# Kernel optimization log

Hardware: AMD Instinct MI355X
Metric: run time of the kernel (lower is better)

Reference implementation:

```python
import jax, jax.numpy as jnp
import numpy as np

NEG = -10000.0
PAD_ID = 0


def setup_inputs() -> dict:
    key = jax.random.key(0)
    ks = jax.random.split(key, 9)
    B, S, D, K, L = 32, 256, 512, 8, 64
    word_rep = jax.random.normal(ks[0], (B, S, D), jnp.float32)
    mask = jnp.ones((B, S), jnp.int32)
    # conv_w[k,:,:,:k+1] are the taps of Conv1d(D, D, k+1); padded to width K for a single tensor
    conv_w = jax.random.normal(ks[1], (K, D, D, K), jnp.float32) * 0.02
    conv_b = jax.random.normal(ks[2], (K, D), jnp.float32) * 0.02
    cls_w = jax.random.normal(ks[3], (L, D), jnp.float32) * 0.02
    cls_b = jax.random.normal(ks[4], (L,), jnp.float32) * 0.02
    T = jax.random.normal(ks[5], (L, L), jnp.float32) * 0.01
    T = T.at[PAD_ID, :].set(NEG).at[:, PAD_ID].set(NEG)
    T_from_BEGIN = jax.random.normal(ks[6], (L,), jnp.float32) * 0.01
    T_from_BEGIN = T_from_BEGIN.at[PAD_ID].set(NEG)
    T_to_END = jax.random.normal(ks[7], (L,), jnp.float32) * 0.01
    T_to_END = T_to_END.at[PAD_ID].set(NEG)
    return dict(word_rep=word_rep, mask=mask, conv_w=conv_w, conv_b=conv_b,
                cls_w=cls_w, cls_b=cls_b, T=T, T_from_BEGIN=T_from_BEGIN, T_to_END=T_to_END)


def _semicrf(word_rep, mask, conv_w, conv_b, cls_w, cls_b, T, T_from_BEGIN, T_to_END):
    B, S, D = word_rep.shape
    K = conv_w.shape[0]
    L = cls_w.shape[0]
    # ---- segment representations: Conv1d(D, D, k+1) placed at [:, k:, k, :] ----
    x = jnp.transpose(word_rep, (0, 2, 1))  # [B, D, S]
    word_seq_rep = jnp.zeros((B, S, K, D), word_rep.dtype)
    for k in range(K):
        w = conv_w[k, :, :, :k + 1]  # [D_out, D_in, k+1]
        out = jax.lax.conv_general_dilated(
            x, w, window_strides=(1,), padding='VALID',
            dimension_numbers=('NCH', 'OIH', 'NCH')) + conv_b[k][None, :, None]  # [B, D, S-k]
        word_seq_rep = word_seq_rep.at[:, k:, k, :].set(jnp.transpose(out, (0, 2, 1)))
    # ---- label scores ----
    label_score = jnp.einsum('bskd,ld->bskl', word_seq_rep, cls_w) + cls_b  # [B,S,K,L]
    label_score = label_score.at[..., PAD_ID].set(NEG)
    seg_ok = jnp.arange(K)[None, :] <= jnp.arange(S)[:, None]  # [S, K]: segment of len k+1 valid only if t >= k
    mask3 = (mask[:, :, None] == 1) & seg_ok[None]              # [B, S, K]
    label_score = jnp.where(mask3[..., None], label_score, NEG)
    # ---- semi-CRF forward recursion over t (sequential scan) ----
    # buf[:, j] holds log_alpha at position t-1-j for j in [0, K)
    def step(buf, inp):
        ls_t, m_t, t = inp  # [B,K,L], [B,K], scalar
        lse_prev = jax.nn.logsumexp(buf, axis=2)                                  # over kk -> [B,K,L']
        tmp = jax.nn.logsumexp(T[None, None, :, :] + lse_prev[:, :, None, :], axis=3)  # over l' -> [B,K,L]
        rec = jnp.where(m_t[..., None], ls_t + tmp, NEG)
        begin = ls_t + T_from_BEGIN[None, None, :]
        karr = jnp.arange(K)[None, :, None]
        row = jnp.where(karr == t, begin, jnp.where(karr > t, NEG, rec))  # [B,K,L]
        buf = jnp.concatenate([row[:, None], buf[:, :-1]], axis=1)
        return buf, row

    buf0 = jnp.full((B, K, K, L), NEG, word_rep.dtype)
    xs = (jnp.transpose(label_score, (1, 0, 2, 3)), jnp.transpose(mask3, (1, 0, 2)), jnp.arange(S))
    _, rows = jax.lax.scan(step, buf0, xs)
    log_alpha = jnp.concatenate(
        [jnp.transpose(rows, (1, 0, 2, 3)), jnp.full((B, 1, K, L), NEG, word_rep.dtype)], axis=1)  # [B,S+1,K,L]
    # ---- log partition: gather log_alpha at last token per segment length, add T_to_END, logsumexp ----
    lengths = jnp.sum(mask, axis=1)                                   # [B]
    idxs = lengths[:, None] - (jnp.arange(K)[None, :] + 1)            # [B,K]
    idxs = jnp.where(idxs >= 0, idxs, S - 1)
    idx_arr = jnp.broadcast_to(idxs[:, None, :, None], (B, 1, K, L))
    g = jnp.take_along_axis(log_alpha, idx_arr, axis=1)[:, 0]         # [B,K,L]
    scores = g + T_to_END[None, None, :]
    return jax.nn.logsumexp(scores.reshape(B, K * L), axis=1)         # [B]


def reference(word_rep, mask, conv_w, conv_b, cls_w, cls_b, T, T_from_BEGIN, T_to_END):
    return _semicrf(word_rep, mask, conv_w, conv_b, cls_w, cls_b, T, T_from_BEGIN, T_to_END)
```

## Files before the change

### kernel.cpp

```cpp
#include <hip/hip_runtime.h>
#include <hip/hip_bf16.h>

#define NEGV (-10000.0f)
constexpr int B_ = 32, S_ = 256, D_ = 512, K_ = 8, L_ = 64;

typedef __bf16 bf16_t;
typedef bf16_t bf16x8 __attribute__((ext_vector_type(8)));
typedef float f32x4 __attribute__((ext_vector_type(4)));

__device__ __forceinline__ float u2f(unsigned int u) {
  union { unsigned int u; float f; } x; x.u = u; return x.f;
}
__device__ __forceinline__ unsigned int f2bfbits(float f) {
  union { bf16_t h; unsigned short u; } x; x.h = (bf16_t)f; return (unsigned int)x.u;
}

__global__ __launch_bounds__(256) void cast_kernel(const float* __restrict__ wr,
                                                   bf16_t* __restrict__ Awr,
                                                   const float* __restrict__ cls_w,
                                                   bf16_t* __restrict__ clsb) {
  const int bid = blockIdx.x;
  if (bid < 2048) {
    const int i = (bid * 256 + threadIdx.x) * 8;
    const float4 a = *(const float4*)(wr + i);
    const float4 b = *(const float4*)(wr + i + 4);
    bf16x8 o;
    o[0] = (bf16_t)a.x; o[1] = (bf16_t)a.y; o[2] = (bf16_t)a.z; o[3] = (bf16_t)a.w;
    o[4] = (bf16_t)b.x; o[5] = (bf16_t)b.y; o[6] = (bf16_t)b.z; o[7] = (bf16_t)b.w;
    *(bf16x8*)(Awr + i) = o;
  } else {
    const int i = ((bid - 2048) * 256 + threadIdx.x) * 8;
    const float4 a = *(const float4*)(cls_w + i);
    const float4 b = *(const float4*)(cls_w + i + 4);
    bf16x8 o;
    o[0] = (bf16_t)a.x; o[1] = (bf16_t)a.y; o[2] = (bf16_t)a.z; o[3] = (bf16_t)a.w;
    o[4] = (bf16_t)b.x; o[5] = (bf16_t)b.y; o[6] = (bf16_t)b.z; o[7] = (bf16_t)b.w;
    *(bf16x8*)(clsb + i) = o;
  }
}

__global__ __launch_bounds__(256) void w2_kernel(const float* __restrict__ conv_w,
                                                 const bf16_t* __restrict__ clsb,
                                                 bf16_t* __restrict__ Vt) {
  const int k = blockIdx.y;
  const int m0 = blockIdx.x * 128;
  const int tid = threadIdx.x;
  const int w = tid >> 6, lane = tid & 63;
  const int wm = w & 1, wn = w >> 1;
  const int lrow = lane & 15, quad = lane >> 4;
  const float* A = conv_w + (size_t)k * 2097152;
  f32x4 acc[4][2] = {};
#pragma unroll 2
  for (int kk = 0; kk < 16; kk++) {
    const int d0 = kk * 32 + quad * 8;
    const bf16x8 b0 = *(const bf16x8*)(clsb + (wn * 32 + lrow) * 512 + kk * 32 + quad * 8);
    const bf16x8 b1 = *(const bf16x8*)(clsb + (wn * 32 + 16 + lrow) * 512 + kk * 32 + quad * 8);
#pragma unroll
    for (int mi = 0; mi < 4; mi++) {
      const int ih = m0 + wm * 64 + mi * 16 + lrow;
      const float* ap = A + (size_t)d0 * 4096 + ih;
      bf16x8 a;
      a[0] = (bf16_t)ap[0 * 4096]; a[1] = (bf16_t)ap[1 * 4096];
      a[2] = (bf16_t)ap[2 * 4096]; a[3] = (bf16_t)ap[3 * 4096];
      a[4] = (bf16_t)ap[4 * 4096]; a[5] = (bf16_t)ap[5 * 4096];
      a[6] = (bf16_t)ap[6 * 4096]; a[7] = (bf16_t)ap[7 * 4096];
      acc[mi][0] = __builtin_amdgcn_mfma_f32_16x16x32_bf16(a, b0, acc[mi][0], 0, 0, 0);
      acc[mi][1] = __builtin_amdgcn_mfma_f32_16x16x32_bf16(a, b1, acc[mi][1], 0, 0, 0);
    }
  }
#pragma unroll
  for (int mi = 0; mi < 4; mi++) {
#pragma unroll
    for (int dd = 0; dd < 4; dd++) {
      const int ih = m0 + wm * 64 + mi * 16 + quad * 4 + dd;
      const int i = ih >> 3, h = ih & 7;
      const int o = k - h;
      if (o >= 0) {
#pragma unroll
        for (int ni = 0; ni < 2; ni++) {
          const int l = wn * 32 + ni * 16 + lrow;
          Vt[(size_t)(k * 64 + l) * 4096 + o * 512 + i] = (bf16_t)acc[mi][ni][dd];
        }
      }
    }
  }
}

__global__ __launch_bounds__(256) void bias2_kernel(const float* __restrict__ conv_b,
                                                    const float* __restrict__ cls_w,
                                                    const float* __restrict__ cls_b,
                                                    float* __restrict__ bias2) {
  const int k = blockIdx.x;
  const int tid = threadIdx.x;
  const int l = tid & 63, c = tid >> 6;
  __shared__ float partb[4][64];
  float s = 0.f;
  for (int d = c * 128; d < c * 128 + 128; d++)
    s += conv_b[k * D_ + d] * cls_w[l * D_ + d];
  partb[c][l] = s;
  __syncthreads();
  if (tid < 64)
    bias2[k * 64 + tid] = cls_b[tid] + partb[0][tid] + partb[1][tid] + partb[2][tid] + partb[3][tid];
}

__global__ __launch_bounds__(256) void ls_mfma(const bf16_t* __restrict__ Awr,
                                               const bf16_t* __restrict__ Vt,
                                               const float* __restrict__ bias2,
                                               const int* __restrict__ mask,
                                               unsigned int* __restrict__ ELSd) {
  constexpr int LDA = 520;
  __shared__ __align__(16) bf16_t As[71 * LDA];
  const int tid = threadIdx.x;
  const int m0 = blockIdx.x * 64;
  const int y = blockIdx.y;
  const int w = tid >> 6, lane = tid & 63;
  const int lrow = lane & 15, quad = lane >> 4;
  const int tblA[4] = {7, 0, 5, 2}, tblB[4] = {6, 1, 4, 3};
  const int kS = (y == 0) ? tblA[w] : tblB[w];

  for (int c = tid; c < 71 * 64; c += 256) {
    const int row = c >> 6, col8 = c & 63;
    int src = m0 - 7 + row;
    if (src < 0) src = 0;
    const uint4 v = *(const uint4*)(Awr + (size_t)src * 512 + col8 * 8);
    *(uint4*)(&As[row * LDA + col8 * 8]) = v;
  }
  __syncthreads();

  f32x4 acc[4][4] = {};
  const int NJ = 16 * (kS + 1);
  const bf16_t* vbase = Vt + (size_t)(kS * 64 + lrow) * 4096 + quad * 8;
#pragma unroll 2
  for (int j = 0; j < NJ; j++) {
    const int o = j >> 4;
    const int col = (j & 15) * 32;
    bf16x8 bfr[4];
#pragma unroll
    for (int ni = 0; ni < 4; ni++)
      bfr[ni] = *(const bf16x8*)(vbase + (size_t)(ni * 16) * 4096 + j * 32);
    const int abase = (lrow + 7 - o) * LDA + col + quad * 8;
#pragma unroll
    for (int mi = 0; mi < 4; mi++) {
      const bf16x8 a = *(const bf16x8*)(&As[abase + mi * 16 * LDA]);
#pragma unroll
      for (int ni = 0; ni < 4; ni++)
        acc[mi][ni] = __builtin_amdgcn_mfma_f32_16x16x32_bf16(a, bfr[ni], acc[mi][ni], 0, 0, 0);
    }
  }

  __syncthreads();
  unsigned short* buf = (unsigned short*)As;
#pragma unroll
  for (int ni = 0; ni < 4; ni++) {
    const int l = ni * 16 + lrow;
    const float bn = bias2[kS * 64 + l];
#pragma unroll
    for (int mi = 0; mi < 4; mi++) {
#pragma unroll
      for (int d = 0; d < 4; d++) {
        const int ml = mi * 16 + quad * 4 + d;
        const int m = m0 + ml;
        const int t = m & 255;
        const bool mok = (mask[m] == 1) && (t >= kS) && (l != 0);
        const float e = mok ? __expf(acc[mi][ni][d] + bn) : 0.f;
        buf[w * 4096 + ml * 64 + l] = (unsigned short)f2bfbits(e);
      }
    }
  }
  __syncthreads();
#pragma unroll
  for (int g = 0; g < 2; g++) {
    const int plane = g * 2 + y;
    const unsigned short* lo = buf + (g * 2) * 4096;
    const unsigned short* hi = buf + (g * 2 + 1) * 4096;
#pragma unroll
    for (int it = 0; it < 16; it++) {
      const int idx = it * 256 + tid;
      const unsigned int dw = (unsigned int)lo[idx] | ((unsigned int)hi[idx] << 16);
      ELSd[((size_t)plane * 8192 + m0 + (idx >> 6)) * 64 + (idx & 63)] = dw;
    }
  }
}

__global__ __launch_bounds__(64) void dp_kernel(const float* __restrict__ T,
                                                const float* __restrict__ Tfb_g,
                                                const unsigned int* __restrict__ ELSd,
                                                float* __restrict__ Mg_lin,
                                                float* __restrict__ cs_g) {
  const int b = blockIdx.x;
  const int l = threadIdx.x;
  __shared__ __align__(16) float ebuf[64];

  f32x4 rTv[16];
#pragma unroll
  for (int jj = 0; jj < 16; jj++) {
    const float4 tv = *(const float4*)(T + l * 64 + jj * 4);
    rTv[jj][0] = __expf(tv.x);
    rTv[jj][1] = __expf(tv.y);
    rTv[jj][2] = __expf(tv.z);
    rTv[jj][3] = __expf(tv.w);
  }

  const unsigned int* e0p = ELSd + ((size_t)0 * 8192 + b * 256) * 64 + l;
  const unsigned int* e1p = ELSd + ((size_t)1 * 8192 + b * 256) * 64 + l;
  const unsigned int* e2p = ELSd + ((size_t)2 * 8192 + b * 256) * 64 + l;
  const unsigned int* e3p = ELSd + ((size_t)3 * 8192 + b * 256) * 64 + l;

  float mh0 = __expf(Tfb_g[l]);
  float mh1 = 0.f, mh2 = 0.f, mh3 = 0.f, mh4 = 0.f, mh5 = 0.f, mh6 = 0.f, mh7 = 0.f;
  float c = 0.f;
  float m4 = 0.f;
  float S_next = 0.f;

  uint4 r0 = make_uint4(e0p[0 * 64], e1p[0 * 64], e2p[0 * 64], e3p[0 * 64]);
  uint4 r1 = make_uint4(e0p[1 * 64], e1p[1 * 64], e2p[1 * 64], e3p[1 * 64]);
  uint4 r2 = make_uint4(e0p[2 * 64], e1p[2 * 64], e2p[2 * 64], e3p[2 * 64]);
  uint4 r3 = make_uint4(e0p[3 * 64], e1p[3 * 64], e2p[3 * 64], e3p[3 * 64]);

  for (int t4 = 0; t4 < 256; t4 += 4) {
#pragma unroll
    for (int u = 0; u < 4; u++) {
      const int t = t4 + u;
      if (t > 0) {
        if ((t & 3) == 0) {
          const float S = fmaxf(S_next, 1e-30f);
          const float inv = __builtin_amdgcn_rcpf(S);
          c += __logf(S);
          mh7 = mh6 * inv; mh6 = mh5 * inv; mh5 = mh4 * inv; mh4 = mh3 * inv;
          mh3 = mh2 * inv; mh2 = mh1 * inv; mh1 = mh0 * inv; mh0 = m4 * inv;
        } else {
          mh7 = mh6; mh6 = mh5; mh5 = mh4; mh4 = mh3;
          mh3 = mh2; mh2 = mh1; mh1 = mh0; mh0 = m4;
        }
      }
      const uint4 q = (u == 0) ? r0 : (u == 1) ? r1 : (u == 2) ? r2 : r3;
      const float f7 = u2f(q.x << 16), fk0 = u2f(q.x & 0xFFFF0000u);
      const float f6 = u2f(q.y << 16), fk1 = u2f(q.y & 0xFFFF0000u);
      const float f5 = u2f(q.z << 16), fk2 = u2f(q.z & 0xFFFF0000u);
      const float f4 = u2f(q.w << 16), fk3 = u2f(q.w & 0xFFFF0000u);
      const float e = ((fk0 * mh0 + fk1 * mh1) + (fk2 * mh2 + fk3 * mh3)) +
                      ((f4 * mh4 + f5 * mh5) + (f6 * mh6 + f7 * mh7));
      ebuf[l] = e;
      asm volatile("s_waitcnt lgkmcnt(0)" ::: "memory");

      {
        int nt = t + 4;
        if (nt > 255) nt = 255;
        const uint4 nv = make_uint4(e0p[(size_t)nt * 64], e1p[(size_t)nt * 64],
                                    e2p[(size_t)nt * 64], e3p[(size_t)nt * 64]);
        if (u == 0) r0 = nv; else if (u == 1) r1 = nv; else if (u == 2) r2 = nv; else r3 = nv;
      }
      if ((t & 3) == 3) {
        float pm = e;
#pragma unroll
        for (int off = 32; off > 0; off >>= 1) pm = fmaxf(pm, __shfl_xor(pm, off));
        S_next = pm;
      }

      f32x4 acc = {0.f, 0.f, 0.f, 0.f};
      const f32x4* ev = (const f32x4*)ebuf;
#pragma unroll
      for (int jj = 0; jj < 16; jj++) acc += rTv[jj] * ev[jj];
      m4 = (acc[0] + acc[1]) + (acc[2] + acc[3]);

      Mg_lin[((size_t)b * 256 + t) * 64 + l] = m4;
      if (l == 0) cs_g[b * 256 + t] = c;
    }
  }
}

__global__ __launch_bounds__(64) void final_kernel(const int* __restrict__ mask,
                                                   const float* __restrict__ Tfb_g,
                                                   const float* __restrict__ T2e_g,
                                                   const unsigned int* __restrict__ ELSd,
                                                   const float* __restrict__ Mg_lin,
                                                   const float* __restrict__ cs_g,
                                                   float* __restrict__ out) {
  const int b = blockIdx.x, lane = threadIdx.x;
  int lenp = 0;
  for (int s = lane; s < S_; s += 64) lenp += (mask[b * S_ + s] == 1) ? 1 : 0;
#pragma unroll
  for (int off = 32; off > 0; off >>= 1) lenp += __shfl_xor(lenp, off);
  const int len = lenp;
  const float t2e = T2e_g[lane];
  float vals[8];
  float mx = -3.4e38f;
#pragma unroll
  for (int k = 0; k < 8; k++) {
    int tk = len - 1 - k;
    if (tk < 0) tk = S_ - 1;
    float g;
    if (k > tk) {
      g = NEGV;
    } else {
      const int p = (k < 4) ? k : (7 - k);
      const unsigned int dw = ELSd[((size_t)p * 8192 + b * 256 + tk) * 64 + lane];
      const float elsv = (k < 4) ? u2f(dw & 0xFFFF0000u) : u2f(dw << 16);
      const float ls = (elsv > 0.f) ? __logf(elsv) : NEGV;
      if (k == tk) {
        g = ls + Tfb_g[lane];
      } else if (mask[b * S_ + tk] == 1) {
        const int u = tk - 1 - k;
        const float mlin = Mg_lin[((size_t)b * S_ + u) * 64 + lane];
        const float M = (mlin > 0.f) ? (__logf(mlin) + cs_g[b * S_ + u]) : -1e30f;
        g = ls + M;
      } else {
        g = NEGV;
      }
    }
    const float v = g + t2e;
    vals[k] = v;
    mx = fmaxf(mx, v);
  }
#pragma unroll
  for (int off = 32; off > 0; off >>= 1) mx = fmaxf(mx, __shfl_xor(mx, off));
  float s = 0.f;
#pragma unroll
  for (int k = 0; k < 8; k++) s += __expf(vals[k] - mx);
#pragma unroll
  for (int off = 32; off > 0; off >>= 1) s += __shfl_xor(s, off);
  if (lane == 0) out[b] = __logf(s) + mx;
}

extern "C" void kernel_launch(void* const* d_in, const int* in_sizes, int n_in,
                              void* d_out, int out_size, void* d_ws, size_t ws_size,
                              hipStream_t stream) {
  const float* wr     = (const float*)d_in[0];
  const int*   mask   = (const int*)d_in[1];
  const float* conv_w = (const float*)d_in[2];
  const float* conv_b = (const float*)d_in[3];
  const float* cls_w  = (const float*)d_in[4];
  const float* cls_b  = (const float*)d_in[5];
  const float* T      = (const float*)d_in[6];
  const float* Tfb    = (const float*)d_in[7];
  const float* T2e    = (const float*)d_in[8];
  float* out = (float*)d_out;

  float* ws = (float*)d_ws;
  bf16_t* Vt    = (bf16_t*)ws;
  bf16_t* Awr   = (bf16_t*)(ws + 1048576);
  float*  bias2 = ws + 3145728;
  unsigned int* ELSd = (unsigned int*)(ws + 3146240);
  float*  Mg    = ws + 5243392;
  float*  cs    = ws + 5767680;
  bf16_t* clsb  = (bf16_t*)(ws + 5775872);

  cast_kernel<<<2064, 256, 0, stream>>>(wr, Awr, cls_w, clsb);
  w2_kernel<<<dim3(32, 8), 256, 0, stream>>>(conv_w, clsb, Vt);
  bias2_kernel<<<8, 256, 0, stream>>>(conv_b, cls_w, cls_b, bias2);
  ls_mfma<<<dim3(128, 2), 256, 0, stream>>>(Awr, Vt, bias2, mask, ELSd);
  dp_kernel<<<32, 64, 0, stream>>>(T, Tfb, ELSd, Mg, cs);
  final_kernel<<<32, 64, 0, stream>>>(mask, Tfb, T2e, ELSd, Mg, cs, out);
}
```

Before: 307.4 us.

## Interleave two batch DP recurrences per wavefront to hide step latency

The semi-CRF forward recurrence kernel now processes two batch elements per 64-thread block, interleaving their per-step decode, LDS exchange, and T-matrix accumulation so that one chain's latency can overlap the other's. The grid shrinks from 32 to 16 blocks, with separate LDS buffers for each chain. This trades parallelism across compute units for instruction-level parallelism within a wave, and it raises register pressure.

Result: slower. 393.2 us (+27.9%).

```diff
diff --git a/kernel.cpp b/kernel.cpp
--- a/kernel.cpp
+++ b/kernel.cpp
@@ -182,14 +182,62 @@
   }
 }
 
-__global__ __launch_bounds__(64) void dp_kernel(const float* __restrict__ T,
-                                                const float* __restrict__ Tfb_g,
-                                                const unsigned int* __restrict__ ELSd,
-                                                float* __restrict__ Mg_lin,
-                                                float* __restrict__ cs_g) {
-  const int b = blockIdx.x;
+#define DP_SHIFT_RESCALE(P)                                                  \
+  {                                                                          \
+    const float S = fmaxf(P##S, 1e-30f);                                     \
+    const float inv = __builtin_amdgcn_rcpf(S);                              \
+    P##c += __logf(S);                                                       \
+    P##mh7 = P##mh6 * inv; P##mh6 = P##mh5 * inv;                            \
+    P##mh5 = P##mh4 * inv; P##mh4 = P##mh3 * inv;                            \
+    P##mh3 = P##mh2 * inv; P##mh2 = P##mh1 * inv;                            \
+    P##mh1 = P##mh0 * inv; P##mh0 = P##m4 * inv;                             \
+  }
+
+#define DP_SHIFT_PLAIN(P)                                                    \
+  {                                                                          \
+    P##mh7 = P##mh6; P##mh6 = P##mh5; P##mh5 = P##mh4; P##mh4 = P##mh3;      \
+    P##mh3 = P##mh2; P##mh2 = P##mh1; P##mh1 = P##mh0; P##mh0 = P##m4;       \
+  }
+
+#define DP_DECODE_WRITE(P, q, eb)                                            \
+  {                                                                          \
+    const float f7 = u2f((q).x << 16), fk0 = u2f((q).x & 0xFFFF0000u);       \
+    const float f6 = u2f((q).y << 16), fk1 = u2f((q).y & 0xFFFF0000u);       \
+    const float f5 = u2f((q).z << 16), fk2 = u2f((q).z & 0xFFFF0000u);       \
+    const float f4 = u2f((q).w << 16), fk3 = u2f((q).w & 0xFFFF0000u);       \
+    P##e = ((fk0 * P##mh0 + fk1 * P##mh1) + (fk2 * P##mh2 + fk3 * P##mh3)) + \
+           ((f4 * P##mh4 + f5 * P##mh5) + (f6 * P##mh6 + f7 * P##mh7));      \
+    (eb)[l] = P##e;                                                          \
+  }
+
+#define DP_PHASE2(P, q, eb, t, u)                                            \
+  {                                                                          \
+    int nt = (t) + 4; if (nt > 255) nt = 255;                                \
+    q = make_uint4(P##e0[(size_t)nt * 64], P##e1[(size_t)nt * 64],           \
+                   P##e2[(size_t)nt * 64], P##e3[(size_t)nt * 64]);          \
+    if ((u) == 3) {                                                          \
+      float pm = P##e;                                                       \
+      pm = fmaxf(pm, __shfl_xor(pm, 32)); pm = fmaxf(pm, __shfl_xor(pm, 16));\
+      pm = fmaxf(pm, __shfl_xor(pm, 8));  pm = fmaxf(pm, __shfl_xor(pm, 4)); \
+      pm = fmaxf(pm, __shfl_xor(pm, 2));  pm = fmaxf(pm, __shfl_xor(pm, 1)); \
+      P##S = pm;                                                             \
+    }                                                                        \
+    f32x4 acc = {0.f, 0.f, 0.f, 0.f};                                        \
+    const f32x4* ev = (const f32x4*)(eb);                                    \
+    _Pragma("unroll")                                                        \
+    for (int jj = 0; jj < 16; jj++) acc += rTv[jj] * ev[jj];                 \
+    P##m4 = (acc[0] + acc[1]) + (acc[2] + acc[3]);                           \
+    Mg_lin[((size_t)P##b * 256 + (t)) * 64 + l] = P##m4;                     \
+    if (l == 0) cs_g[P##b * 256 + (t)] = P##c;                               \
+  }
+
+__global__ __launch_bounds__(64, 1) void dp_kernel(const float* __restrict__ T,
+                                                   const float* __restrict__ Tfb_g,
+                                                   const unsigned int* __restrict__ ELSd,
+                                                   float* __restrict__ Mg_lin,
+                                                   float* __restrict__ cs_g) {
   const int l = threadIdx.x;
-  __shared__ __align__(16) float ebuf[64];
+  __shared__ __align__(16) float ebuf2[2][64];
 
   f32x4 rTv[16];
 #pragma unroll
@@ -200,72 +248,60 @@
     rTv[jj][2] = __expf(tv.z);
     rTv[jj][3] = __expf(tv.w);
   }
-
-  const unsigned int* e0p = ELSd + ((size_t)0 * 8192 + b * 256) * 64 + l;
-  const unsigned int* e1p = ELSd + ((size_t)1 * 8192 + b * 256) * 64 + l;
-  const unsigned int* e2p = ELSd + ((size_t)2 * 8192 + b * 256) * 64 + l;
-  const unsigned int* e3p = ELSd + ((size_t)3 * 8192 + b * 256) * 64 + l;
-
-  float mh0 = __expf(Tfb_g[l]);
-  float mh1 = 0.f, mh2 = 0.f, mh3 = 0.f, mh4 = 0.f, mh5 = 0.f, mh6 = 0.f, mh7 = 0.f;
-  float c = 0.f;
-  float m4 = 0.f;
-  float S_next = 0.f;
-
-  uint4 r0 = make_uint4(e0p[0 * 64], e1p[0 * 64], e2p[0 * 64], e3p[0 * 64]);
-  uint4 r1 = make_uint4(e0p[1 * 64], e1p[1 * 64], e2p[1 * 64], e3p[1 * 64]);
-  uint4 r2 = make_uint4(e0p[2 * 64], e1p[2 * 64], e2p[2 * 64], e3p[2 * 64]);
-  uint4 r3 = make_uint4(e0p[3 * 64], e1p[3 * 64], e2p[3 * 64], e3p[3 * 64]);
+  const float mh0init = __expf(Tfb_g[l]);
+
+  const int Ab = blockIdx.x;
+  const int Bb = blockIdx.x + 16;
+  const unsigned int* Ae0 = ELSd + ((size_t)0 * 8192 + Ab * 256) * 64 + l;
+  const unsigned int* Ae1 = Ae0 + (size_t)8192 * 64;
+  const unsigned int* Ae2 = Ae1 + (size_t)8192 * 64;
+  const unsigned int* Ae3 = Ae2 + (size_t)8192 * 64;
+  const unsigned int* Be0 = ELSd + ((size_t)0 * 8192 + Bb * 256) * 64 + l;
+  const unsigned int* Be1 = Be0 + (size_t)8192 * 64;
+  const unsigned int* Be2 = Be1 + (size_t)8192 * 64;
+  const unsigned int* Be3 = Be2 + (size_t)8192 * 64;
+
+  float Amh0 = mh0init, Amh1 = 0.f, Amh2 = 0.f, Amh3 = 0.f,
+        Amh4 = 0.f, Amh5 = 0.f, Amh6 = 0.f, Amh7 = 0.f;
+  float Bmh0 = mh0init, Bmh1 = 0.f, Bmh2 = 0.f, Bmh3 = 0.f,
+        Bmh4 = 0.f, Bmh5 = 0.f, Bmh6 = 0.f, Bmh7 = 0.f;
+  float Ac = 0.f, Bc = 0.f, Am4 = 0.f, Bm4 = 0.f, AS = 0.f, BS = 0.f;
+  float Ae = 0.f, Be = 0.f;
+
+  uint4 Ar0 = make_uint4(Ae0[0], Ae1[0], Ae2[0], Ae3[0]);
+  uint4 Ar1 = make_uint4(Ae0[64], Ae1[64], Ae2[64], Ae3[64]);
+  uint4 Ar2 = make_uint4(Ae0[128], Ae1[128], Ae2[128], Ae3[128]);
+  uint4 Ar3 = make_uint4(Ae0[192], Ae1[192], Ae2[192], Ae3[192]);
+  uint4 Br0 = make_uint4(Be0[0], Be1[0], Be2[0], Be3[0]);
+  uint4 Br1 = make_uint4(Be0[64], Be1[64], Be2[64], Be3[64]);
+  uint4 Br2 = make_uint4(Be0[128], Be1[128], Be2[128], Be3[128]);
+  uint4 Br3 = make_uint4(Be0[192], Be1[192], Be2[192], Be3[192]);
 
   for (int t4 = 0; t4 < 256; t4 += 4) {
-#pragma unroll
-    for (int u = 0; u < 4; u++) {
-      const int t = t4 + u;
-      if (t > 0) {
-        if ((t & 3) == 0) {
-          const float S = fmaxf(S_next, 1e-30f);
-          const float inv = __builtin_amdgcn_rcpf(S);
-          c += __logf(S);
-          mh7 = mh6 * inv; mh6 = mh5 * inv; mh5 = mh4 * inv; mh4 = mh3 * inv;
-          mh3 = mh2 * inv; mh2 = mh1 * inv; mh1 = mh0 * inv; mh0 = m4 * inv;
-        } else {
-          mh7 = mh6; mh6 = mh5; mh5 = mh4; mh4 = mh3;
-          mh3 = mh2; mh2 = mh1; mh1 = mh0; mh0 = m4;
-        }
-      }
-      const uint4 q = (u == 0) ? r0 : (u == 1) ? r1 : (u == 2) ? r2 : r3;
-      const float f7 = u2f(q.x << 16), fk0 = u2f(q.x & 0xFFFF0000u);
-      const float f6 = u2f(q.y << 16), fk1 = u2f(q.y & 0xFFFF0000u);
-      const float f5 = u2f(q.z << 16), fk2 = u2f(q.z & 0xFFFF0000u);
-      const float f4 = u2f(q.w << 16), fk3 = u2f(q.w & 0xFFFF0000u);
-      const float e = ((fk0 * mh0 + fk1 * mh1) + (fk2 * mh2 + fk3 * mh3)) +
-                      ((f4 * mh4 + f5 * mh5) + (f6 * mh6 + f7 * mh7));
-      ebuf[l] = e;
-      asm volatile("s_waitcnt lgkmcnt(0)" ::: "memory");
-
-      {
-        int nt = t + 4;
-        if (nt > 255) nt = 255;
-        const uint4 nv = make_uint4(e0p[(size_t)nt * 64], e1p[(size_t)nt * 64],
-                                    e2p[(size_t)nt * 64], e3p[(size_t)nt * 64]);
-        if (u == 0) r0 = nv; else if (u == 1) r1 = nv; else if (u == 2) r2 = nv; else r3 = nv;
-      }
-      if ((t & 3) == 3) {
-        float pm = e;
-#pragma unroll
-        for (int off = 32; off > 0; off >>= 1) pm = fmaxf(pm, __shfl_xor(pm, off));
-        S_next = pm;
-      }
-
-      f32x4 acc = {0.f, 0.f, 0.f, 0.f};
-      const f32x4* ev = (const f32x4*)ebuf;
-#pragma unroll
-      for (int jj = 0; jj < 16; jj++) acc += rTv[jj] * ev[jj];
-      m4 = (acc[0] + acc[1]) + (acc[2] + acc[3]);
-
-      Mg_lin[((size_t)b * 256 + t) * 64 + l] = m4;
-      if (l == 0) cs_g[b * 256 + t] = c;
-    }
+    if (t4 > 0) { DP_SHIFT_RESCALE(A); DP_SHIFT_RESCALE(B); }
+    DP_DECODE_WRITE(A, Ar0, ebuf2[0]);
+    DP_DECODE_WRITE(B, Br0, ebuf2[1]);
+    asm volatile("s_waitcnt lgkmcnt(0)" ::: "memory");
+    DP_PHASE2(A, Ar0, ebuf2[0], t4 + 0, 0);
+    DP_PHASE2(B, Br0, ebuf2[1], t4 + 0, 0);
+    DP_SHIFT_PLAIN(A); DP_SHIFT_PLAIN(B);
+    DP_DECODE_WRITE(A, Ar1, ebuf2[0]);
+    DP_DECODE_WRITE(B, Br1, ebuf2[1]);
+    asm volatile("s_waitcnt lgkmcnt(0)" ::: "memory");
+    DP_PHASE2(A, Ar1, ebuf2[0], t4 + 1, 1);
+    DP_PHASE2(B, Br1, ebuf2[1], t4 + 1, 1);
+    DP_SHIFT_PLAIN(A); DP_SHIFT_PLAIN(B);
+    DP_DECODE_WRITE(A, Ar2, ebuf2[0]);
+    DP_DECODE_WRITE(B, Br2, ebuf2[1]);
+    asm volatile("s_waitcnt lgkmcnt(0)" ::: "memory");
+    DP_PHASE2(A, Ar2, ebuf2[0], t4 + 2, 2);
+    DP_PHASE2(B, Br2, ebuf2[1], t4 + 2, 2);
+    DP_SHIFT_PLAIN(A); DP_SHIFT_PLAIN(B);
+    DP_DECODE_WRITE(A, Ar3, ebuf2[0]);
+    DP_DECODE_WRITE(B, Br3, ebuf2[1]);
+    asm volatile("s_waitcnt lgkmcnt(0)" ::: "memory");
+    DP_PHASE2(A, Ar3, ebuf2[0], t4 + 3, 3);
+    DP_PHASE2(B, Br3, ebuf2[1], t4 + 3, 3);
   }
 }
 
@@ -349,6 +385,6 @@
   w2_kernel<<<dim3(32, 8), 256, 0, stream>>>(conv_w, clsb, Vt);
   bias2_kernel<<<8, 256, 0, stream>>>(conv_b, cls_w, cls_b, bias2);
   ls_mfma<<<dim3(128, 2), 256, 0, stream>>>(Awr, Vt, bias2, mask, ELSd);
-  dp_kernel<<<32, 64, 0, stream>>>(T, Tfb, ELSd, Mg, cs);
+  dp_kernel<<<16, 64, 0, stream>>>(T, Tfb, ELSd, Mg, cs);
   final_kernel<<<32, 64, 0, stream>>>(mask, Tfb, T2e, ELSd, Mg, cs, out);
 }
```

## Replace LDS broadcast in DP recurrence with DPP row rotations and shuffles

Applied to the files above, without the earlier changes.

The per-timestep 64x64 matvec in the semi-CRF forward DP no longer writes the emission vector to LDS and reads it back. Each lane now obtains the other quarters via three __shfl calls and rotates values within 16-lane rows using DPP row_ror, with the exp(T) registers pre-permuted to match the rotation order. The normalizer also changes from a max-reduction to a rotation-accumulated sum, which avoids the separate xor-shuffle reduction. This aims to shorten the serial latency of each of the 256 dependent steps, at the cost of 64 DPP moves per step and a different, still valid, scaling choice.

Result: no change. 313.1 us (+1.8%).

```diff
diff --git a/kernel.cpp b/kernel.cpp
--- a/kernel.cpp
+++ b/kernel.cpp
@@ -13,6 +13,12 @@
 }
 __device__ __forceinline__ unsigned int f2bfbits(float f) {
   union { bf16_t h; unsigned short u; } x; x.h = (bf16_t)f; return (unsigned int)x.u;
+}
+__device__ __forceinline__ float row_ror1(float x) {
+  union { float f; int i; } a, r;
+  a.f = x;
+  r.i = __builtin_amdgcn_update_dpp(a.i, a.i, 0x121, 0xF, 0xF, false);
+  return r.f;
 }
 
 __global__ __launch_bounds__(256) void cast_kernel(const float* __restrict__ wr,
@@ -182,24 +188,24 @@
   }
 }
 
-__global__ __launch_bounds__(64) void dp_kernel(const float* __restrict__ T,
-                                                const float* __restrict__ Tfb_g,
-                                                const unsigned int* __restrict__ ELSd,
-                                                float* __restrict__ Mg_lin,
-                                                float* __restrict__ cs_g) {
+__global__ __launch_bounds__(64, 1) void dp_kernel(const float* __restrict__ T,
+                                                   const float* __restrict__ Tfb_g,
+                                                   const unsigned int* __restrict__ ELSd,
+                                                   float* __restrict__ Mg_lin,
+                                                   float* __restrict__ cs_g) {
   const int b = blockIdx.x;
   const int l = threadIdx.x;
-  __shared__ __align__(16) float ebuf[64];
-
-  f32x4 rTv[16];
-#pragma unroll
-  for (int jj = 0; jj < 16; jj++) {
-    const float4 tv = *(const float4*)(T + l * 64 + jj * 4);
-    rTv[jj][0] = __expf(tv.x);
-    rTv[jj][1] = __expf(tv.y);
-    rTv[jj][2] = __expf(tv.z);
-    rTv[jj][3] = __expf(tv.w);
-  }
+
+  const float* Trow = T + l * 64;
+#define TE(Q, I) __expf(Trow[((((l & 48) | ((l - (I)) & 15)) + 16 * (Q)) & 63)])
+#define MKT(VAR, Q, C) \
+  const f32x4 VAR = { TE(Q, (C)*4 + 0), TE(Q, (C)*4 + 1), TE(Q, (C)*4 + 2), TE(Q, (C)*4 + 3) };
+  MKT(tA0, 0, 0) MKT(tA1, 0, 1) MKT(tA2, 0, 2) MKT(tA3, 0, 3)
+  MKT(tB0, 1, 0) MKT(tB1, 1, 1) MKT(tB2, 1, 2) MKT(tB3, 1, 3)
+  MKT(tC0, 2, 0) MKT(tC1, 2, 1) MKT(tC2, 2, 2) MKT(tC3, 2, 3)
+  MKT(tD0, 3, 0) MKT(tD1, 3, 1) MKT(tD2, 3, 2) MKT(tD3, 3, 3)
+#undef MKT
+#undef TE
 
   const unsigned int* e0p = ELSd + ((size_t)0 * 8192 + b * 256) * 64 + l;
   const unsigned int* e1p = ELSd + ((size_t)1 * 8192 + b * 256) * 64 + l;
@@ -212,61 +218,88 @@
   float m4 = 0.f;
   float S_next = 0.f;
 
+  const int lq1 = (l + 16) & 63, lq2 = (l + 32) & 63, lq3 = (l + 48) & 63;
+
   uint4 r0 = make_uint4(e0p[0 * 64], e1p[0 * 64], e2p[0 * 64], e3p[0 * 64]);
   uint4 r1 = make_uint4(e0p[1 * 64], e1p[1 * 64], e2p[1 * 64], e3p[1 * 64]);
   uint4 r2 = make_uint4(e0p[2 * 64], e1p[2 * 64], e2p[2 * 64], e3p[2 * 64]);
   uint4 r3 = make_uint4(e0p[3 * 64], e1p[3 * 64], e2p[3 * 64], e3p[3 * 64]);
 
+#define RND(TA, TB, TC, TD, E) \
+  a0 += TA[E] * v0; a1 += TB[E] * v1; a2 += TC[E] * v2; a3 += TD[E] * v3;
+#define RNDS(TA, TB, TC, TD, E)                         \
+  a0 += TA[E] * v0; s0 += v0; a1 += TB[E] * v1; s1 += v1; \
+  a2 += TC[E] * v2; s2 += v2; a3 += TD[E] * v3; s3 += v3;
+#define ROT \
+  v0 = row_ror1(v0); v1 = row_ror1(v1); v2 = row_ror1(v2); v3 = row_ror1(v3);
+
+#define DP_STEP(U, RQ)                                                          \
+  {                                                                             \
+    const int t = t4 + (U);                                                     \
+    if ((U) == 0) {                                                             \
+      if (t4 > 0) {                                                             \
+        const float S = fmaxf(S_next, 1e-30f);                                  \
+        const float inv = __builtin_amdgcn_rcpf(S);                             \
+        c += __logf(S);                                                         \
+        mh7 = mh6 * inv; mh6 = mh5 * inv; mh5 = mh4 * inv; mh4 = mh3 * inv;     \
+        mh3 = mh2 * inv; mh2 = mh1 * inv; mh1 = mh0 * inv; mh0 = m4 * inv;      \
+      }                                                                         \
+    } else {                                                                    \
+      mh7 = mh6; mh6 = mh5; mh5 = mh4; mh4 = mh3;                               \
+      mh3 = mh2; mh2 = mh1; mh1 = mh0; mh0 = m4;                                \
+    }                                                                           \
+    const float f7 = u2f(RQ.x << 16), fk0 = u2f(RQ.x & 0xFFFF0000u);            \
+    const float f6 = u2f(RQ.y << 16), fk1 = u2f(RQ.y & 0xFFFF0000u);            \
+    const float f5 = u2f(RQ.z << 16), fk2 = u2f(RQ.z & 0xFFFF0000u);            \
+    const float f4 = u2f(RQ.w << 16), fk3 = u2f(RQ.w & 0xFFFF0000u);            \
+    const float e = ((fk0 * mh0 + fk1 * mh1) + (fk2 * mh2 + fk3 * mh3)) +       \
+                    ((f4 * mh4 + f5 * mh5) + (f6 * mh6 + f7 * mh7));            \
+    const float eb1 = __shfl(e, lq1);                                           \
+    const float eb2 = __shfl(e, lq2);                                           \
+    const float eb3 = __shfl(e, lq3);                                           \
+    {                                                                           \
+      int nt = t + 4; if (nt > 255) nt = 255;                                   \
+      RQ = make_uint4(e0p[(size_t)nt * 64], e1p[(size_t)nt * 64],               \
+                      e2p[(size_t)nt * 64], e3p[(size_t)nt * 64]);              \
+    }                                                                           \
+    float a0 = 0.f, a1 = 0.f, a2 = 0.f, a3 = 0.f;                               \
+    float v0 = e, v1 = eb1, v2 = eb2, v3 = eb3;                                 \
+    if ((U) == 3) {                                                             \
+      float s0 = 0.f, s1 = 0.f, s2 = 0.f, s3 = 0.f;                             \
+      RNDS(tA0, tB0, tC0, tD0, 0) ROT RNDS(tA0, tB0, tC0, tD0, 1) ROT           \
+      RNDS(tA0, tB0, tC0, tD0, 2) ROT RNDS(tA0, tB0, tC0, tD0, 3) ROT           \
+      RNDS(tA1, tB1, tC1, tD1, 0) ROT RNDS(tA1, tB1, tC1, tD1, 1) ROT           \
+      RNDS(tA1, tB1, tC1, tD1, 2) ROT RNDS(tA1, tB1, tC1, tD1, 3) ROT           \
+      RNDS(tA2, tB2, tC2, tD2, 0) ROT RNDS(tA2, tB2, tC2, tD2, 1) ROT           \
+      RNDS(tA2, tB2, tC2, tD2, 2) ROT RNDS(tA2, tB2, tC2, tD2, 3) ROT           \
+      RNDS(tA3, tB3, tC3, tD3, 0) ROT RNDS(tA3, tB3, tC3, tD3, 1) ROT           \
+      RNDS(tA3, tB3, tC3, tD3, 2) ROT RNDS(tA3, tB3, tC3, tD3, 3)               \
+      S_next = (s0 + s1) + (s2 + s3);                                           \
+    } else {                                                                    \
+      RND(tA0, tB0, tC0, tD0, 0) ROT RND(tA0, tB0, tC0, tD0, 1) ROT             \
+      RND(tA0, tB0, tC0, tD0, 2) ROT RND(tA0, tB0, tC0, tD0, 3) ROT             \
+      RND(tA1, tB1, tC1, tD1, 0) ROT RND(tA1, tB1, tC1, tD1, 1) ROT             \
+      RND(tA1, tB1, tC1, tD1, 2) ROT RND(tA1, tB1, tC1, tD1, 3) ROT             \
+      RND(tA2, tB2, tC2, tD2, 0) ROT RND(tA2, tB2, tC2, tD2, 1) ROT             \
+      RND(tA2, tB2, tC2, tD2, 2) ROT RND(tA2, tB2, tC2, tD2, 3) ROT             \
+      RND(tA3, tB3, tC3, tD3, 0) ROT RND(tA3, tB3, tC3, tD3, 1) ROT             \
+      RND(tA3, tB3, tC3, tD3, 2) ROT RND(tA3, tB3, tC3, tD3, 3)                 \
+    }                                                                           \
+    m4 = (a0 + a1) + (a2 + a3);                                                 \
+    Mg_lin[((size_t)b * 256 + t) * 64 + l] = m4;                                \
+    if (l == 0) cs_g[b * 256 + t] = c;                                          \
+  }
+
   for (int t4 = 0; t4 < 256; t4 += 4) {
-#pragma unroll
-    for (int u = 0; u < 4; u++) {
-      const int t = t4 + u;
-      if (t > 0) {
-        if ((t & 3) == 0) {
-          const float S = fmaxf(S_next, 1e-30f);
-          const float inv = __builtin_amdgcn_rcpf(S);
-          c += __logf(S);
-          mh7 = mh6 * inv; mh6 = mh5 * inv; mh5 = mh4 * inv; mh4 = mh3 * inv;
-          mh3 = mh2 * inv; mh2 = mh1 * inv; mh1 = mh0 * inv; mh0 = m4 * inv;
-        } else {
-          mh7 = mh6; mh6 = mh5; mh5 = mh4; mh4 = mh3;
-          mh3 = mh2; mh2 = mh1; mh1 = mh0; mh0 = m4;
-        }
-      }
-      const uint4 q = (u == 0) ? r0 : (u == 1) ? r1 : (u == 2) ? r2 : r3;
-      const float f7 = u2f(q.x << 16), fk0 = u2f(q.x & 0xFFFF0000u);
-      const float f6 = u2f(q.y << 16), fk1 = u2f(q.y & 0xFFFF0000u);
-      const float f5 = u2f(q.z << 16), fk2 = u2f(q.z & 0xFFFF0000u);
-      const float f4 = u2f(q.w << 16), fk3 = u2f(q.w & 0xFFFF0000u);
-      const float e = ((fk0 * mh0 + fk1 * mh1) + (fk2 * mh2 + fk3 * mh3)) +
-                      ((f4 * mh4 + f5 * mh5) + (f6 * mh6 + f7 * mh7));
-      ebuf[l] = e;
-      asm volatile("s_waitcnt lgkmcnt(0)" ::: "memory");
-
-      {
-        int nt = t + 4;
-        if (nt > 255) nt = 255;
-        const uint4 nv = make_uint4(e0p[(size_t)nt * 64], e1p[(size_t)nt * 64],
-                                    e2p[(size_t)nt * 64], e3p[(size_t)nt * 64]);
-        if (u == 0) r0 = nv; else if (u == 1) r1 = nv; else if (u == 2) r2 = nv; else r3 = nv;
-      }
-      if ((t & 3) == 3) {
-        float pm = e;
-#pragma unroll
-        for (int off = 32; off > 0; off >>= 1) pm = fmaxf(pm, __shfl_xor(pm, off));
-        S_next = pm;
-      }
-
-      f32x4 acc = {0.f, 0.f, 0.f, 0.f};
-      const f32x4* ev = (const f32x4*)ebuf;
-#pragma unroll
-      for (int jj = 0; jj < 16; jj++) acc += rTv[jj] * ev[jj];
-      m4 = (acc[0] + acc[1]) + (acc[2] + acc[3]);
-
-      Mg_lin[((size_t)b * 256 + t) * 64 + l] = m4;
-      if (l == 0) cs_g[b * 256 + t] = c;
-    }
-  }
+    DP_STEP(0, r0)
+    DP_STEP(1, r1)
+    DP_STEP(2, r2)
+    DP_STEP(3, r3)
+  }
+#undef DP_STEP
+#undef RND
+#undef RNDS
+#undef ROT
 }
 
 __global__ __launch_bounds__(64) void final_kernel(const int* __restrict__ mask,
```

## Restructure DP recurrence to shorten serial chain and fold bias kernel into w2

Applied to the files above, without the earlier changes.

The serial per-batch DP loop is reordered so the partial dot product for the next step's emission term is computed ahead of time. Only the newest m4 term then sits on the critical path. The per-block max-shuffle reduction used for rescaling becomes a sum over the shared ebuf, computed during the same LDS reads, and the explicit lgkmcnt wait is dropped. The bias2 kernel is merged into w2_kernel (block x==0) to save one launch. Rescaling by sum instead of max changes numerics slightly, and removing the explicit wait relies on compiler ordering of the LDS write and read.

New measurement: 288.0 us. 6.3% less time.

```diff
diff --git a/kernel.cpp b/kernel.cpp
--- a/kernel.cpp
+++ b/kernel.cpp
@@ -41,7 +41,11 @@
 
 __global__ __launch_bounds__(256) void w2_kernel(const float* __restrict__ conv_w,
                                                  const bf16_t* __restrict__ clsb,
-                                                 bf16_t* __restrict__ Vt) {
+                                                 bf16_t* __restrict__ Vt,
+                                                 const float* __restrict__ conv_b,
+                                                 const float* __restrict__ cls_w,
+                                                 const float* __restrict__ cls_b,
+                                                 float* __restrict__ bias2) {
   const int k = blockIdx.y;
   const int m0 = blockIdx.x * 128;
   const int tid = threadIdx.x;
@@ -84,23 +88,17 @@
       }
     }
   }
-}
-
-__global__ __launch_bounds__(256) void bias2_kernel(const float* __restrict__ conv_b,
-                                                    const float* __restrict__ cls_w,
-                                                    const float* __restrict__ cls_b,
-                                                    float* __restrict__ bias2) {
-  const int k = blockIdx.x;
-  const int tid = threadIdx.x;
-  const int l = tid & 63, c = tid >> 6;
-  __shared__ float partb[4][64];
-  float s = 0.f;
-  for (int d = c * 128; d < c * 128 + 128; d++)
-    s += conv_b[k * D_ + d] * cls_w[l * D_ + d];
-  partb[c][l] = s;
-  __syncthreads();
-  if (tid < 64)
-    bias2[k * 64 + tid] = cls_b[tid] + partb[0][tid] + partb[1][tid] + partb[2][tid] + partb[3][tid];
+  if (blockIdx.x == 0) {
+    __shared__ float partb[4][64];
+    const int bl = tid & 63, bc = tid >> 6;
+    float s = 0.f;
+    for (int d = bc * 128; d < bc * 128 + 128; d++)
+      s += conv_b[k * D_ + d] * cls_w[bl * D_ + d];
+    partb[bc][bl] = s;
+    __syncthreads();
+    if (tid < 64)
+      bias2[k * 64 + tid] = cls_b[tid] + partb[0][tid] + partb[1][tid] + partb[2][tid] + partb[3][tid];
+  }
 }
 
 __global__ __launch_bounds__(256) void ls_mfma(const bf16_t* __restrict__ Awr,
@@ -217,56 +215,73 @@
   uint4 r2 = make_uint4(e0p[2 * 64], e1p[2 * 64], e2p[2 * 64], e3p[2 * 64]);
   uint4 r3 = make_uint4(e0p[3 * 64], e1p[3 * 64], e2p[3 * 64], e3p[3 * 64]);
 
+  float e = u2f(r0.x & 0xFFFF0000u) * mh0;
+
+#define DP_STEP(U, RQ, RN)                                                      \
+  {                                                                             \
+    const int t = t4 + (U);                                                     \
+    ebuf[l] = e;                                                                \
+                    \
+    const float nf7 = u2f(RN.x << 16), nk0 = u2f(RN.x & 0xFFFF0000u);           \
+    const float nf6 = u2f(RN.y << 16), nk1 = u2f(RN.y & 0xFFFF0000u);           \
+    const float nf5 = u2f(RN.z << 16), nk2 = u2f(RN.z & 0xFFFF0000u);           \
+    const float nf4 = u2f(RN.w << 16), nk3 = u2f(RN.w & 0xFFFF0000u);           \
+    const float pe = ((nk1 * mh0 + nk2 * mh1) + (nk3 * mh2 + nf4 * mh3)) +      \
+                     ((nf5 * mh4 + nf6 * mh5) + nf7 * mh6);                     \
+                                                  \
+    {                                                                           \
+      int nt = t + 4; if (nt > 255) nt = 255;                                   \
+      RQ = make_uint4(e0p[(size_t)nt * 64], e1p[(size_t)nt * 64],               \
+                      e2p[(size_t)nt * 64], e3p[(size_t)nt * 64]);              \
+    }                                                                           \
+                                     \
+    const f32x4* ev = (const f32x4*)ebuf;                                       \
+    f32x4 A0 = {0.f, 0.f, 0.f, 0.f}, A1 = {0.f, 0.f, 0.f, 0.f};                 \
+    f32x4 A2 = {0.f, 0.f, 0.f, 0.f}, A3 = {0.f, 0.f, 0.f, 0.f};                 \
+    if ((U) == 3) {                                                             \
+      f32x4 s0 = {0.f, 0.f, 0.f, 0.f}, s1 = {0.f, 0.f, 0.f, 0.f};               \
+      _Pragma("unroll")                                                         \
+      for (int jj = 0; jj < 4; jj++) {                                          \
+        const f32x4 v0 = ev[jj], v1 = ev[4 + jj], v2 = ev[8 + jj], v3 = ev[12 + jj]; \
+        A0 += rTv[jj] * v0; A1 += rTv[4 + jj] * v1;                             \
+        A2 += rTv[8 + jj] * v2; A3 += rTv[12 + jj] * v3;                        \
+        s0 += v0 + v2; s1 += v1 + v3;                                           \
+      }                                                                         \
+      const f32x4 ss = s0 + s1;                                                 \
+      S_next = (ss[0] + ss[1]) + (ss[2] + ss[3]);                               \
+    } else {                                                                    \
+      _Pragma("unroll")                                                         \
+      for (int jj = 0; jj < 4; jj++) {                                          \
+        A0 += rTv[jj] * ev[jj]; A1 += rTv[4 + jj] * ev[4 + jj];                 \
+        A2 += rTv[8 + jj] * ev[8 + jj]; A3 += rTv[12 + jj] * ev[12 + jj];       \
+      }                                                                         \
+    }                                                                           \
+    const f32x4 As4 = (A0 + A1) + (A2 + A3);                                    \
+    m4 = (As4[0] + As4[1]) + (As4[2] + As4[3]);                                 \
+    Mg_lin[((size_t)b * 256 + t) * 64 + l] = m4;                                \
+    if (l == 0) cs_g[b * 256 + t] = c;                                          \
+     \
+    if ((U) == 3) {                                                             \
+      const float S = fmaxf(S_next, 1e-30f);                                    \
+      const float inv = __builtin_amdgcn_rcpf(S);                               \
+      c += __logf(S);                                                           \
+      mh7 = mh6 * inv; mh6 = mh5 * inv; mh5 = mh4 * inv; mh4 = mh3 * inv;       \
+      mh3 = mh2 * inv; mh2 = mh1 * inv; mh1 = mh0 * inv; mh0 = m4 * inv;        \
+      e = inv * (nk0 * m4 + pe);                                                \
+    } else {                                                                    \
+      mh7 = mh6; mh6 = mh5; mh5 = mh4; mh4 = mh3;                               \
+      mh3 = mh2; mh2 = mh1; mh1 = mh0; mh0 = m4;                                \
+      e = nk0 * m4 + pe;                                                        \
+    }                                                                           \
+  }
+
   for (int t4 = 0; t4 < 256; t4 += 4) {
-#pragma unroll
-    for (int u = 0; u < 4; u++) {
-      const int t = t4 + u;
-      if (t > 0) {
-        if ((t & 3) == 0) {
-          const float S = fmaxf(S_next, 1e-30f);
-          const float inv = __builtin_amdgcn_rcpf(S);
-          c += __logf(S);
-          mh7 = mh6 * inv; mh6 = mh5 * inv; mh5 = mh4 * inv; mh4 = mh3 * inv;
-          mh3 = mh2 * inv; mh2 = mh1 * inv; mh1 = mh0 * inv; mh0 = m4 * inv;
-        } else {
-          mh7 = mh6; mh6 = mh5; mh5 = mh4; mh4 = mh3;
-          mh3 = mh2; mh2 = mh1; mh1 = mh0; mh0 = m4;
-        }
-      }
-      const uint4 q = (u == 0) ? r0 : (u == 1) ? r1 : (u == 2) ? r2 : r3;
-      const float f7 = u2f(q.x << 16), fk0 = u2f(q.x & 0xFFFF0000u);
-      const float f6 = u2f(q.y << 16), fk1 = u2f(q.y & 0xFFFF0000u);
-      const float f5 = u2f(q.z << 16), fk2 = u2f(q.z & 0xFFFF0000u);
-      const float f4 = u2f(q.w << 16), fk3 = u2f(q.w & 0xFFFF0000u);
-      const float e = ((fk0 * mh0 + fk1 * mh1) + (fk2 * mh2 + fk3 * mh3)) +
-                      ((f4 * mh4 + f5 * mh5) + (f6 * mh6 + f7 * mh7));
-      ebuf[l] = e;
-      asm volatile("s_waitcnt lgkmcnt(0)" ::: "memory");
-
-      {
-        int nt = t + 4;
-        if (nt > 255) nt = 255;
-        const uint4 nv = make_uint4(e0p[(size_t)nt * 64], e1p[(size_t)nt * 64],
-                                    e2p[(size_t)nt * 64], e3p[(size_t)nt * 64]);
-        if (u == 0) r0 = nv; else if (u == 1) r1 = nv; else if (u == 2) r2 = nv; else r3 = nv;
-      }
-      if ((t & 3) == 3) {
-        float pm = e;
-#pragma unroll
-        for (int off = 32; off > 0; off >>= 1) pm = fmaxf(pm, __shfl_xor(pm, off));
-        S_next = pm;
-      }
-
-      f32x4 acc = {0.f, 0.f, 0.f, 0.f};
-      const f32x4* ev = (const f32x4*)ebuf;
-#pragma unroll
-      for (int jj = 0; jj < 16; jj++) acc += rTv[jj] * ev[jj];
-      m4 = (acc[0] + acc[1]) + (acc[2] + acc[3]);
-
-      Mg_lin[((size_t)b * 256 + t) * 64 + l] = m4;
-      if (l == 0) cs_g[b * 256 + t] = c;
-    }
-  }
+    DP_STEP(0, r0, r1)
+    DP_STEP(1, r1, r2)
+    DP_STEP(2, r2, r3)
+    DP_STEP(3, r3, r0)
+  }
+#undef DP_STEP
 }
 
 __global__ __launch_bounds__(64) void final_kernel(const int* __restrict__ mask,
@@ -346,8 +361,7 @@
   bf16_t* clsb  = (bf16_t*)(ws + 5775872);
 
   cast_kernel<<<2064, 256, 0, stream>>>(wr, Awr, cls_w, clsb);
-  w2_kernel<<<dim3(32, 8), 256, 0, stream>>>(conv_w, clsb, Vt);
-  bias2_kernel<<<8, 256, 0, stream>>>(conv_b, cls_w, cls_b, bias2);
+  w2_kernel<<<dim3(32, 8), 256, 0, stream>>>(conv_w, clsb, Vt, conv_b, cls_w, cls_b, bias2);
   ls_mfma<<<dim3(128, 2), 256, 0, stream>>>(Awr, Vt, bias2, mask, ELSd);
   dp_kernel<<<32, 64, 0, stream>>>(T, Tfb, ELSd, Mg, cs);
   final_kernel<<<32, 64, 0, stream>>>(mask, Tfb, T2e, ELSd, Mg, cs, out);
```
